# Kernel tuning notes

Measured on AMD Instinct MI355X. Metric: run time of the kernel, lower is better.

## Reference

```python
import jax, jax.numpy as jnp
import numpy as np

N_NODES = 100000
N_EDGES = 1600000
D_IN = 128
D_HID = 128
D_OUT = 2
N_GRAPHS = 1024


def setup_inputs() -> dict:
    key = jax.random.key(0)
    ks = jax.random.split(key, 10)
    x = jax.random.normal(ks[0], (N_NODES, D_IN), dtype=jnp.float32)
    edge_index = jax.random.randint(ks[1], (2, N_EDGES), 0, N_NODES, dtype=jnp.int64)
    batch = jnp.sort(jax.random.randint(ks[2], (N_NODES,), 0, N_GRAPHS, dtype=jnp.int64))
    s = 1.0 / np.sqrt(D_IN)
    W1 = jax.random.uniform(ks[3], (D_IN, D_HID), jnp.float32, -s, s)
    b1 = jnp.zeros((D_HID,), jnp.float32)
    W2 = jax.random.uniform(ks[4], (D_HID, D_HID), jnp.float32, -s, s)
    b2 = jnp.zeros((D_HID,), jnp.float32)
    Wc = jax.random.uniform(ks[5], (D_HID, D_OUT), jnp.float32, -s, s)
    bc = jnp.zeros((D_OUT,), jnp.float32)
    return {"x": x, "edge_index": edge_index, "batch": batch,
            "W1": W1, "b1": b1, "W2": W2, "b2": b2, "Wc": Wc, "bc": bc}


def reference(x, edge_index, batch, W1, b1, W2, b2, Wc, bc):
    N = x.shape[0]
    # GCNConv: add self-loops, symmetric normalization D^-1/2 A D^-1/2
    loops = jnp.arange(N, dtype=edge_index.dtype)
    src = jnp.concatenate([edge_index[0], loops])
    dst = jnp.concatenate([edge_index[1], loops])
    deg = jax.ops.segment_sum(jnp.ones_like(dst, dtype=x.dtype), dst, num_segments=N)
    dinv = jnp.where(deg > 0, jax.lax.rsqrt(jnp.maximum(deg, 1e-12)), 0.0)
    norm = (dinv[src] * dinv[dst])[:, None]  # [E+N, 1]

    def gcn_conv(h, W, b):
        h = h @ W                                  # linear (no bias in PyG lin)
        msg = h[src] * norm                        # gather + scale
        agg = jax.ops.segment_sum(msg, dst, num_segments=N)  # scatter-add
        return agg + b

    h = jax.nn.relu(gcn_conv(x, W1, b1))   # dropout: inference mode (identity)
    h = jax.nn.relu(gcn_conv(h, W2, b2))
    # global_mean_pool over graph ids
    sums = jax.ops.segment_sum(h, batch, num_segments=N_GRAPHS)
    cnts = jax.ops.segment_sum(jnp.ones((N,), h.dtype), batch, num_segments=N_GRAPHS)
    pooled = sums / jnp.maximum(cnts, 1.0)[:, None]
    return pooled @ Wc + bc
```

## Files before the change

kernel.cpp:

```cpp
#include <hip/hip_runtime.h>

#define NN 100000
#define NE 1600000
#define D 128
#define NG 1024
#define SCAN_CHUNK 2048
#define NB ((NN + SCAN_CHUNK - 1) / SCAN_CHUNK)
#define GEMM_BLKS ((NN + 63) / 64)
#define HIST_BLKS ((NE + 255) / 256)
#define BOUNDS_BLKS 5

typedef _Float16 h4 __attribute__((ext_vector_type(4)));

template<int RELU, typename TIN>
__device__ __forceinline__ void gemm_body(const TIN* __restrict__ in,
                                          const float* __restrict__ W,
                                          const float* __restrict__ bias_in,
                                          _Float16* __restrict__ out,
                                          int blk) {
    __shared__ float xs[2][16][68];
    __shared__ float ws[2][16][128];

    int tid  = threadIdx.x;
    int row0 = blk * 64;

    int srow = tid >> 2;
    int skq  = (tid & 3) * 4;
    int wkr  = tid >> 5;
    int wcq  = (tid & 31) * 4;
    int tx = tid & 15, ty = tid >> 4;
    int r0 = ty * 4, c0 = tx * 4;

    float4 lx, lw0, lw1;

    auto LOAD = [&](int kp) {
        int k0 = kp * 16;
        int rg = row0 + srow; if (rg >= NN) rg = NN - 1;
        const TIN* rp = in + (size_t)rg * D + k0 + skq;
        if constexpr (sizeof(TIN) == 4) {
            lx = *(const float4*)rp;
        } else {
            h4 hv = *(const h4*)rp;
            lx = make_float4((float)hv.x, (float)hv.y, (float)hv.z, (float)hv.w);
        }
        lw0 = *(const float4*)(W + (size_t)(k0 + wkr) * D + wcq);
        lw1 = *(const float4*)(W + (size_t)(k0 + 8 + wkr) * D + wcq);
        if (RELU) {
            float4 bb = *(const float4*)(bias_in + k0 + skq);
            lx.x = fmaxf(lx.x + bb.x, 0.f);
            lx.y = fmaxf(lx.y + bb.y, 0.f);
            lx.z = fmaxf(lx.z + bb.z, 0.f);
            lx.w = fmaxf(lx.w + bb.w, 0.f);
        }
    };
    auto WRITE = [&](int buf) {
        xs[buf][skq + 0][srow] = lx.x;
        xs[buf][skq + 1][srow] = lx.y;
        xs[buf][skq + 2][srow] = lx.z;
        xs[buf][skq + 3][srow] = lx.w;
        *(float4*)&ws[buf][wkr][wcq]     = lw0;
        *(float4*)&ws[buf][wkr + 8][wcq] = lw1;
    };

    float acc[4][8] = {};

    LOAD(0);
    WRITE(0);
    __syncthreads();

    for (int kp = 0; kp < 8; ++kp) {
        int cur = kp & 1;
        if (kp < 7) LOAD(kp + 1);
#pragma unroll
        for (int kk = 0; kk < 16; ++kk) {
            float4 xa = *(const float4*)&xs[cur][kk][r0];
            float4 wa = *(const float4*)&ws[cur][kk][c0];
            float4 wb = *(const float4*)&ws[cur][kk][c0 + 64];
            float xv[4] = {xa.x, xa.y, xa.z, xa.w};
            float wv[8] = {wa.x, wa.y, wa.z, wa.w, wb.x, wb.y, wb.z, wb.w};
#pragma unroll
            for (int i = 0; i < 4; ++i)
#pragma unroll
                for (int j = 0; j < 8; ++j)
                    acc[i][j] += xv[i] * wv[j];
        }
        if (kp < 7) {
            WRITE(cur ^ 1);
            __syncthreads();
        }
    }

#pragma unroll
    for (int i = 0; i < 4; ++i) {
        int rg = row0 + r0 + i;
        if (rg < NN) {
            h4 o0 = {(_Float16)acc[i][0], (_Float16)acc[i][1],
                     (_Float16)acc[i][2], (_Float16)acc[i][3]};
            h4 o1 = {(_Float16)acc[i][4], (_Float16)acc[i][5],
                     (_Float16)acc[i][6], (_Float16)acc[i][7]};
            *(h4*)(out + (size_t)rg * D + c0)      = o0;
            *(h4*)(out + (size_t)rg * D + c0 + 64) = o1;
        }
    }
}

__global__ __launch_bounds__(256) void k_gemm1_hist(const float* __restrict__ x,
                                                    const float* __restrict__ W1,
                                                    _Float16* __restrict__ bufA,
                                                    const int* __restrict__ dst,
                                                    int* __restrict__ deg) {
    int b = blockIdx.x;
    if (b < GEMM_BLKS) {
        gemm_body<0, float>(x, W1, nullptr, bufA, b);
    } else {
        int e = (b - GEMM_BLKS) * 256 + threadIdx.x;
        if (e < NE) atomicAdd(&deg[dst[e]], 1);
    }
}

__global__ __launch_bounds__(256) void k_gemm(const _Float16* __restrict__ in,
                                              const float* __restrict__ W,
                                              const float* __restrict__ bias_in,
                                              _Float16* __restrict__ out) {
    gemm_body<1, _Float16>(in, W, bias_in, out, blockIdx.x);
}

__global__ __launch_bounds__(256) void k_scanA(const int* __restrict__ deg,
                                               float* __restrict__ dinv,
                                               int* __restrict__ row_ptr,
                                               int* __restrict__ bsum,
                                               const int* __restrict__ batch,
                                               int* __restrict__ gstart) {
    int b = blockIdx.x, tid = threadIdx.x;
    if (b >= NB) {
        int g = (b - NB) * 256 + tid;
        if (g > NG) return;
        if (g == NG) { gstart[NG] = NN; return; }
        int lo = 0, hi = NN;
        while (lo < hi) {
            int mid = (lo + hi) >> 1;
            if (batch[mid] < g) lo = mid + 1; else hi = mid;
        }
        gstart[g] = lo;
        return;
    }
    __shared__ int sh[256];
    int base = b * SCAN_CHUNK + tid * 8;
    int loc[8];
    int s = 0;
#pragma unroll
    for (int j = 0; j < 8; ++j) {
        int i = base + j;
        int d = (i < NN) ? deg[i] : 0;
        if (i < NN) dinv[i] = rsqrtf((float)(d + 1));
        loc[j] = s;
        s += d;
    }
    sh[tid] = s;
    __syncthreads();
    for (int off = 1; off < 256; off <<= 1) {
        int v = (tid >= off) ? sh[tid - off] : 0;
        __syncthreads();
        sh[tid] += v;
        __syncthreads();
    }
    int excl = (tid == 0) ? 0 : sh[tid - 1];
#pragma unroll
    for (int j = 0; j < 8; ++j) {
        int i = base + j;
        if (i < NN) row_ptr[i] = excl + loc[j];
    }
    if (tid == 255) bsum[b] = sh[255];
}

__global__ __launch_bounds__(256) void k_scanC(int* __restrict__ row_ptr,
                                               const int* __restrict__ bsum,
                                               int* __restrict__ fill) {
    __shared__ int sb[64];
    int tid = threadIdx.x;
    if (tid < NB) sb[tid] = bsum[tid];
    __syncthreads();
    int chunk = (blockIdx.x * 256) / SCAN_CHUNK;
    int pre = 0;
    for (int b = 0; b < chunk; ++b) pre += sb[b];
    int i = blockIdx.x * 256 + tid;
    if (i < NN) {
        int r = row_ptr[i] + pre;
        row_ptr[i] = r;
        fill[i] = r;
    }
    if (i == 0) row_ptr[NN] = NE;
}

__global__ __launch_bounds__(256) void k_fill(const int* __restrict__ src,
                                              const int* __restrict__ dst,
                                              const float* __restrict__ dinv,
                                              int* __restrict__ fill,
                                              int2* __restrict__ csr) {
    int e = blockIdx.x * 256 + threadIdx.x;
    if (e >= NE) return;
    int s = src[e], d = dst[e];
    float nrm = dinv[s] * dinv[d];
    int pos = atomicAdd(&fill[d], 1);
    csr[pos] = make_int2(s, __float_as_int(nrm));
}

__global__ __launch_bounds__(256) void k_gather(const _Float16* __restrict__ hh,
                                                const int* __restrict__ row_ptr,
                                                const int2* __restrict__ csr,
                                                const float* __restrict__ dinv,
                                                _Float16* __restrict__ agg) {
    int t = blockIdx.x * 256 + threadIdx.x;
    int v = t >> 5;
    if (v >= NN) return;
    int c = (t & 31) * 4;

    float di = dinv[v];
    float sl = di * di;
    h4 hv = *(const h4*)(hh + (size_t)v * D + c);
    float4 acc = make_float4((float)hv.x * sl, (float)hv.y * sl,
                             (float)hv.z * sl, (float)hv.w * sl);

    int p   = row_ptr[v];
    int end = row_ptr[v + 1];
    for (; p + 3 < end; p += 4) {
        int2 e0 = csr[p], e1 = csr[p + 1], e2 = csr[p + 2], e3 = csr[p + 3];
        float n0 = __int_as_float(e0.y);
        float n1 = __int_as_float(e1.y);
        float n2 = __int_as_float(e2.y);
        float n3 = __int_as_float(e3.y);
        h4 g0 = *(const h4*)(hh + (size_t)e0.x * D + c);
        h4 g1 = *(const h4*)(hh + (size_t)e1.x * D + c);
        h4 g2 = *(const h4*)(hh + (size_t)e2.x * D + c);
        h4 g3 = *(const h4*)(hh + (size_t)e3.x * D + c);
        acc.x += (float)g0.x * n0; acc.y += (float)g0.y * n0;
        acc.z += (float)g0.z * n0; acc.w += (float)g0.w * n0;
        acc.x += (float)g1.x * n1; acc.y += (float)g1.y * n1;
        acc.z += (float)g1.z * n1; acc.w += (float)g1.w * n1;
        acc.x += (float)g2.x * n2; acc.y += (float)g2.y * n2;
        acc.z += (float)g2.z * n2; acc.w += (float)g2.w * n2;
        acc.x += (float)g3.x * n3; acc.y += (float)g3.y * n3;
        acc.z += (float)g3.z * n3; acc.w += (float)g3.w * n3;
    }
    for (; p < end; ++p) {
        int2 e0 = csr[p];
        float n0 = __int_as_float(e0.y);
        h4 g0 = *(const h4*)(hh + (size_t)e0.x * D + c);
        acc.x += (float)g0.x * n0; acc.y += (float)g0.y * n0;
        acc.z += (float)g0.z * n0; acc.w += (float)g0.w * n0;
    }
    h4 ov = {(_Float16)acc.x, (_Float16)acc.y, (_Float16)acc.z, (_Float16)acc.w};
    *(h4*)(agg + (size_t)v * D + c) = ov;
}

__global__ __launch_bounds__(128) void k_poolcls(const _Float16* __restrict__ agg,
                                                 const float* __restrict__ b2,
                                                 const int* __restrict__ gstart,
                                                 const float* __restrict__ Wc,
                                                 const float* __restrict__ bc,
                                                 float* __restrict__ out) {
    int g = blockIdx.x;
    int c = threadIdx.x;
    int v0 = gstart[g], v1 = gstart[g + 1];
    float bb = b2[c];
    float acc = 0.f;
    int v = v0;
    for (; v + 7 < v1; v += 8) {
        float x0 = (float)agg[(size_t)(v + 0) * D + c];
        float x1 = (float)agg[(size_t)(v + 1) * D + c];
        float x2 = (float)agg[(size_t)(v + 2) * D + c];
        float x3 = (float)agg[(size_t)(v + 3) * D + c];
        float x4 = (float)agg[(size_t)(v + 4) * D + c];
        float x5 = (float)agg[(size_t)(v + 5) * D + c];
        float x6 = (float)agg[(size_t)(v + 6) * D + c];
        float x7 = (float)agg[(size_t)(v + 7) * D + c];
        acc += fmaxf(x0 + bb, 0.f) + fmaxf(x1 + bb, 0.f)
             + fmaxf(x2 + bb, 0.f) + fmaxf(x3 + bb, 0.f)
             + fmaxf(x4 + bb, 0.f) + fmaxf(x5 + bb, 0.f)
             + fmaxf(x6 + bb, 0.f) + fmaxf(x7 + bb, 0.f);
    }
    for (; v < v1; ++v)
        acc += fmaxf((float)agg[(size_t)v * D + c] + bb, 0.f);

    float inv = 1.0f / fmaxf((float)(v1 - v0), 1.0f);
    float pv = acc * inv;

    __shared__ float red[2][128];
    red[0][c] = pv * Wc[c * 2 + 0];
    red[1][c] = pv * Wc[c * 2 + 1];
    __syncthreads();
    if (c < 64) {
        float s = red[0][c] + red[0][c + 64];
        for (int off = 32; off; off >>= 1) s += __shfl_down(s, off);
        if (c == 0) out[g * 2 + 0] = s + bc[0];
    } else {
        int l = c - 64;
        float s = red[1][l] + red[1][l + 64];
        for (int off = 32; off; off >>= 1) s += __shfl_down(s, off);
        if (l == 0) out[g * 2 + 1] = s + bc[1];
    }
}

extern "C" void kernel_launch(void* const* d_in, const int* in_sizes, int n_in,
                              void* d_out, int out_size, void* d_ws, size_t ws_size,
                              hipStream_t stream) {
    const float* x     = (const float*)d_in[0];
    const int*   ei    = (const int*)d_in[1];
    const int*   batch = (const int*)d_in[2];
    const float* W1    = (const float*)d_in[3];
    const float* b1    = (const float*)d_in[4];
    const float* W2    = (const float*)d_in[5];
    const float* b2    = (const float*)d_in[6];
    const float* Wc    = (const float*)d_in[7];
    const float* bc    = (const float*)d_in[8];
    float* out = (float*)d_out;

    const int* src = ei;
    const int* dst = ei + NE;

    char* p = (char*)d_ws;
    int*       deg_i   = (int*)p;       p += 100352 * 4;
    float*     dinv    = (float*)p;     p += 100352 * 4;
    int*       row_ptr = (int*)p;       p += 100352 * 4;
    int*       fillc   = (int*)p;       p += 100352 * 4;
    int*       bsum    = (int*)p;       p += 256 * 4;
    int*       gstart  = (int*)p;       p += 1056 * 4;
    int2*      csr     = (int2*)p;      p += (size_t)NE * 8;
    _Float16*  bufA    = (_Float16*)p;  p += (size_t)NN * D * 2;
    _Float16*  bufB    = (_Float16*)p;  p += (size_t)NN * D * 2;

    hipMemsetAsync(deg_i, 0, 100352 * 4, stream);

    k_gemm1_hist<<<GEMM_BLKS + HIST_BLKS, 256, 0, stream>>>(x, W1, bufA, dst, deg_i);
    k_scanA<<<NB + BOUNDS_BLKS, 256, 0, stream>>>(deg_i, dinv, row_ptr, bsum, batch, gstart);
    k_scanC<<<(NN + 255) / 256, 256, 0, stream>>>(row_ptr, bsum, fillc);
    k_fill<<<HIST_BLKS, 256, 0, stream>>>(src, dst, dinv, fillc, csr);

    k_gather<<<NN * 32 / 256, 256, 0, stream>>>(bufA, row_ptr, csr, dinv, bufB);

    k_gemm<<<GEMM_BLKS, 256, 0, stream>>>(bufB, W2, b1, bufA);
    k_gather<<<NN * 32 / 256, 256, 0, stream>>>(bufA, row_ptr, csr, dinv, bufB);

    k_poolcls<<<NG, 128, 0, stream>>>(bufB, b2, gstart, Wc, bc, out);
}
```

Measured before the change: 377.7 us.

## Replace FP32 SIMT GEMMs with FP16 MFMA GEMMs using pre-transposed weights

The two dense 128x128 GEMMs move from a shared-memory-tiled FP32 FMA kernel to MFMA 16x16x32 f16 instructions. A new prep kernel converts and transposes W1/W2 to fp16, and it also absorbs the degree histogram that used to share a launch with GEMM1. GEMM1 becomes its own launch after the CSR build, and inputs are cast to fp16 before the multiply, which lowers precision. Outputs are written as scalar fp16 stores with a strided pattern, and A operands are loaded directly from global memory without LDS staging.

```diff
diff --git a/kernel.cpp b/kernel.cpp
--- a/kernel.cpp
+++ b/kernel.cpp
@@ -10,119 +10,128 @@
 #define HIST_BLKS ((NE + 255) / 256)
 #define BOUNDS_BLKS 5
 
-typedef _Float16 h4 __attribute__((ext_vector_type(4)));
-
-template<int RELU, typename TIN>
-__device__ __forceinline__ void gemm_body(const TIN* __restrict__ in,
-                                          const float* __restrict__ W,
-                                          const float* __restrict__ bias_in,
+typedef _Float16 h4   __attribute__((ext_vector_type(4)));
+typedef _Float16 h8   __attribute__((ext_vector_type(8)));
+typedef float    f32x4 __attribute__((ext_vector_type(4)));
+
+template<int L2>
+__device__ __forceinline__ void gemm_mfma(const void* __restrict__ inv,
+                                          const _Float16* __restrict__ Wt,
+                                          const float* __restrict__ bias,
                                           _Float16* __restrict__ out,
                                           int blk) {
-    __shared__ float xs[2][16][68];
-    __shared__ float ws[2][16][128];
-
-    int tid  = threadIdx.x;
+    __shared__ _Float16 wl[128][136];
+
+    int tid = threadIdx.x;
+#pragma unroll
+    for (int i = 0; i < 8; ++i) {
+        int s = tid + i * 256;
+        int row = s >> 4, ks = s & 15;
+        *(h8*)&wl[row][ks * 8] = *(const h8*)(Wt + row * D + ks * 8);
+    }
+    __syncthreads();
+
+    int wv = tid >> 6, l = tid & 63;
+    int li = l & 15, lg = l >> 4;
     int row0 = blk * 64;
-
-    int srow = tid >> 2;
-    int skq  = (tid & 3) * 4;
-    int wkr  = tid >> 5;
-    int wcq  = (tid & 31) * 4;
-    int tx = tid & 15, ty = tid >> 4;
-    int r0 = ty * 4, c0 = tx * 4;
-
-    float4 lx, lw0, lw1;
-
-    auto LOAD = [&](int kp) {
-        int k0 = kp * 16;
-        int rg = row0 + srow; if (rg >= NN) rg = NN - 1;
-        const TIN* rp = in + (size_t)rg * D + k0 + skq;
-        if constexpr (sizeof(TIN) == 4) {
-            lx = *(const float4*)rp;
-        } else {
-            h4 hv = *(const h4*)rp;
-            lx = make_float4((float)hv.x, (float)hv.y, (float)hv.z, (float)hv.w);
+    int colw = wv * 32;
+
+    f32x4 acc[4][2] = {};
+
+    const float*    inf = (const float*)inv;
+    const _Float16* inh = (const _Float16*)inv;
+
+#pragma unroll
+    for (int kt = 0; kt < 4; ++kt) {
+        int kb = kt * 32 + lg * 8;
+        float bb[8];
+        if (L2) {
+#pragma unroll
+            for (int e = 0; e < 8; ++e) bb[e] = bias[kb + e];
         }
-        lw0 = *(const float4*)(W + (size_t)(k0 + wkr) * D + wcq);
-        lw1 = *(const float4*)(W + (size_t)(k0 + 8 + wkr) * D + wcq);
-        if (RELU) {
-            float4 bb = *(const float4*)(bias_in + k0 + skq);
-            lx.x = fmaxf(lx.x + bb.x, 0.f);
-            lx.y = fmaxf(lx.y + bb.y, 0.f);
-            lx.z = fmaxf(lx.z + bb.z, 0.f);
-            lx.w = fmaxf(lx.w + bb.w, 0.f);
+        h8 a[4];
+#pragma unroll
+        for (int rt = 0; rt < 4; ++rt) {
+            int rg = row0 + rt * 16 + li; if (rg >= NN) rg = NN - 1;
+            if (L2) {
+                h8 hv = *(const h8*)(inh + (size_t)rg * D + kb);
+                h8 av;
+#pragma unroll
+                for (int e = 0; e < 8; ++e)
+                    av[e] = (_Float16)fmaxf((float)hv[e] + bb[e], 0.f);
+                a[rt] = av;
+            } else {
+                float4 f0 = *(const float4*)(inf + (size_t)rg * D + kb);
+                float4 f1 = *(const float4*)(inf + (size_t)rg * D + kb + 4);
+                h8 av;
+                av[0] = (_Float16)f0.x; av[1] = (_Float16)f0.y;
+                av[2] = (_Float16)f0.z; av[3] = (_Float16)f0.w;
+                av[4] = (_Float16)f1.x; av[5] = (_Float16)f1.y;
+                av[6] = (_Float16)f1.z; av[7] = (_Float16)f1.w;
+                a[rt] = av;
+            }
         }
-    };
-    auto WRITE = [&](int buf) {
-        xs[buf][skq + 0][srow] = lx.x;
-        xs[buf][skq + 1][srow] = lx.y;
-        xs[buf][skq + 2][srow] = lx.z;
-        xs[buf][skq + 3][srow] = lx.w;
-        *(float4*)&ws[buf][wkr][wcq]     = lw0;
-        *(float4*)&ws[buf][wkr + 8][wcq] = lw1;
-    };
-
-    float acc[4][8] = {};
-
-    LOAD(0);
-    WRITE(0);
-    __syncthreads();
-
-    for (int kp = 0; kp < 8; ++kp) {
-        int cur = kp & 1;
-        if (kp < 7) LOAD(kp + 1);
-#pragma unroll
-        for (int kk = 0; kk < 16; ++kk) {
-            float4 xa = *(const float4*)&xs[cur][kk][r0];
-            float4 wa = *(const float4*)&ws[cur][kk][c0];
-            float4 wb = *(const float4*)&ws[cur][kk][c0 + 64];
-            float xv[4] = {xa.x, xa.y, xa.z, xa.w};
-            float wv[8] = {wa.x, wa.y, wa.z, wa.w, wb.x, wb.y, wb.z, wb.w};
-#pragma unroll
-            for (int i = 0; i < 4; ++i)
-#pragma unroll
-                for (int j = 0; j < 8; ++j)
-                    acc[i][j] += xv[i] * wv[j];
+#pragma unroll
+        for (int ct = 0; ct < 2; ++ct) {
+            h8 b = *(const h8*)&wl[colw + ct * 16 + li][kb];
+#pragma unroll
+            for (int rt = 0; rt < 4; ++rt)
+                acc[rt][ct] = __builtin_amdgcn_mfma_f32_16x16x32_f16(
+                    a[rt], b, acc[rt][ct], 0, 0, 0);
         }
-        if (kp < 7) {
-            WRITE(cur ^ 1);
-            __syncthreads();
-        }
-    }
-
-#pragma unroll
-    for (int i = 0; i < 4; ++i) {
-        int rg = row0 + r0 + i;
-        if (rg < NN) {
-            h4 o0 = {(_Float16)acc[i][0], (_Float16)acc[i][1],
-                     (_Float16)acc[i][2], (_Float16)acc[i][3]};
-            h4 o1 = {(_Float16)acc[i][4], (_Float16)acc[i][5],
-                     (_Float16)acc[i][6], (_Float16)acc[i][7]};
-            *(h4*)(out + (size_t)rg * D + c0)      = o0;
-            *(h4*)(out + (size_t)rg * D + c0 + 64) = o1;
-        }
-    }
-}
-
-__global__ __launch_bounds__(256) void k_gemm1_hist(const float* __restrict__ x,
-                                                    const float* __restrict__ W1,
-                                                    _Float16* __restrict__ bufA,
-                                                    const int* __restrict__ dst,
-                                                    int* __restrict__ deg) {
+    }
+
+#pragma unroll
+    for (int rt = 0; rt < 4; ++rt)
+#pragma unroll
+        for (int ct = 0; ct < 2; ++ct)
+#pragma unroll
+            for (int e = 0; e < 4; ++e) {
+                int rg = row0 + rt * 16 + lg * 4 + e;
+                if (rg < NN)
+                    out[(size_t)rg * D + colw + ct * 16 + li] =
+                        (_Float16)acc[rt][ct][e];
+            }
+}
+
+__global__ __launch_bounds__(256) void k_gemm1(const float* __restrict__ x,
+                                               const _Float16* __restrict__ Wt1,
+                                               _Float16* __restrict__ out) {
+    gemm_mfma<0>(x, Wt1, nullptr, out, blockIdx.x);
+}
+
+__global__ __launch_bounds__(256) void k_gemm2(const _Float16* __restrict__ in,
+                                               const _Float16* __restrict__ Wt2,
+                                               const float* __restrict__ b1,
+                                               _Float16* __restrict__ out) {
+    gemm_mfma<1>(in, Wt2, b1, out, blockIdx.x);
+}
+
+__global__ __launch_bounds__(256) void k_pre(const int* __restrict__ dst,
+                                             int* __restrict__ deg,
+                                             const float* __restrict__ W1,
+                                             const float* __restrict__ W2,
+                                             _Float16* __restrict__ Wt1,
+                                             _Float16* __restrict__ Wt2) {
     int b = blockIdx.x;
-    if (b < GEMM_BLKS) {
-        gemm_body<0, float>(x, W1, nullptr, bufA, b);
-    } else {
-        int e = (b - GEMM_BLKS) * 256 + threadIdx.x;
+    if (b < HIST_BLKS) {
+        int e = b * 256 + threadIdx.x;
         if (e < NE) atomicAdd(&deg[dst[e]], 1);
-    }
-}
-
-__global__ __launch_bounds__(256) void k_gemm(const _Float16* __restrict__ in,
-                                              const float* __restrict__ W,
-                                              const float* __restrict__ bias_in,
-                                              _Float16* __restrict__ out) {
-    gemm_body<1, _Float16>(in, W, bias_in, out, blockIdx.x);
+        return;
+    }
+    const float*  W  = (b == HIST_BLKS) ? W1 : W2;
+    _Float16*     Wt = (b == HIST_BLKS) ? Wt1 : Wt2;
+    int t = threadIdx.x;
+#pragma unroll
+    for (int i = 0; i < 16; ++i) {
+        int idx = t + i * 256;
+        int k = idx >> 5, c4 = (idx & 31) * 4;
+        float4 v = *(const float4*)(W + k * D + c4);
+        Wt[(c4 + 0) * D + k] = (_Float16)v.x;
+        Wt[(c4 + 1) * D + k] = (_Float16)v.y;
+        Wt[(c4 + 2) * D + k] = (_Float16)v.z;
+        Wt[(c4 + 3) * D + k] = (_Float16)v.w;
+    }
 }
 
 __global__ __launch_bounds__(256) void k_scanA(const int* __restrict__ deg,
@@ -325,20 +334,23 @@
     int*       fillc   = (int*)p;       p += 100352 * 4;
     int*       bsum    = (int*)p;       p += 256 * 4;
     int*       gstart  = (int*)p;       p += 1056 * 4;
+    _Float16*  Wt1     = (_Float16*)p;  p += 16384 * 2;
+    _Float16*  Wt2     = (_Float16*)p;  p += 16384 * 2;
     int2*      csr     = (int2*)p;      p += (size_t)NE * 8;
     _Float16*  bufA    = (_Float16*)p;  p += (size_t)NN * D * 2;
     _Float16*  bufB    = (_Float16*)p;  p += (size_t)NN * D * 2;
 
     hipMemsetAsync(deg_i, 0, 100352 * 4, stream);
 
-    k_gemm1_hist<<<GEMM_BLKS + HIST_BLKS, 256, 0, stream>>>(x, W1, bufA, dst, deg_i);
+    k_pre<<<HIST_BLKS + 2, 256, 0, stream>>>(dst, deg_i, W1, W2, Wt1, Wt2);
     k_scanA<<<NB + BOUNDS_BLKS, 256, 0, stream>>>(deg_i, dinv, row_ptr, bsum, batch, gstart);
     k_scanC<<<(NN + 255) / 256, 256, 0, stream>>>(row_ptr, bsum, fillc);
     k_fill<<<HIST_BLKS, 256, 0, stream>>>(src, dst, dinv, fillc, csr);
 
+    k_gemm1<<<GEMM_BLKS, 256, 0, stream>>>(x, Wt1, bufA);
     k_gather<<<NN * 32 / 256, 256, 0, stream>>>(bufA, row_ptr, csr, dinv, bufB);
 
-    k_gemm<<<GEMM_BLKS, 256, 0, stream>>>(bufB, W2, b1, bufA);
+    k_gemm2<<<GEMM_BLKS, 256, 0, stream>>>(bufB, Wt2, b1, bufA);
     k_gather<<<NN * 32 / 256, 256, 0, stream>>>(bufA, row_ptr, csr, dinv, bufB);
 
     k_poolcls<<<NG, 128, 0, stream>>>(bufB, b2, gstart, Wc, bc, out);
```

After: 359.5 us, median of 2. 4.8% less time.
